# Performance work log

Hardware: AMD Instinct MI355X
Metric: run time of the kernel (lower is better)

Reference implementation:

```python
import jax, jax.numpy as jnp
import numpy as np

B, L = 32, 512
H, W = 352, 1216
MAXLEN = max(H, W)  # max Bresenham path length after clipping to image


def setup_inputs() -> dict:
    key = jax.random.key(0)
    k1, k2 = jax.random.split(key)
    pred = jax.random.normal(k1, (B, 1, H, W), dtype=jnp.float32)
    lines = jax.random.randint(k2, (B, L, 2, 2), 0, 1216, dtype=jnp.int32)
    return {"pred": pred, "lines": lines}


def _bresenham_paths(lines):
    # lines: [B, L, 2, 2] int32, last dim = (x, y), coords already clipped.
    # Closed-form skimage/Bresenham: along the major axis i=0..dmaj,
    # minor_i = min0 + smin * floor((2*dmin*i + dmaj) / (2*dmaj)).
    x0 = lines[..., 0, 0]; y0 = lines[..., 0, 1]
    x1 = lines[..., 1, 0]; y1 = lines[..., 1, 1]
    dx = jnp.abs(x1 - x0); dy = jnp.abs(y1 - y0)
    xmajor = dx > dy  # skimage 'steep' swap: x is major iff |dx| > |dy|
    dmaj = jnp.where(xmajor, dx, dy)
    dmin = jnp.where(xmajor, dy, dx)
    smaj = jnp.where(xmajor, jnp.sign(x1 - x0), jnp.sign(y1 - y0))
    smin = jnp.where(xmajor, jnp.sign(y1 - y0), jnp.sign(x1 - x0))
    maj0 = jnp.where(xmajor, x0, y0)
    min0 = jnp.where(xmajor, y0, x0)
    i = jnp.arange(MAXLEN, dtype=jnp.int32)
    # Clamp step index to dmaj -> padding repeats the endpoint, so diffs there are 0.
    i_eff = jnp.minimum(i[None, None, :], dmaj[..., None])       # [B, L, MAXLEN]
    dmaj_e = dmaj[..., None]
    dmaj_safe = jnp.maximum(dmaj_e, 1)
    maj = maj0[..., None] + smaj[..., None] * i_eff
    minr = min0[..., None] + smin[..., None] * (
        (2 * dmin[..., None] * i_eff + dmaj_e) // (2 * dmaj_safe))
    xs = jnp.where(xmajor[..., None], maj, minr)
    ys = jnp.where(xmajor[..., None], minr, maj)
    return xs, ys


def reference(pred, lines):
    # Clip coords into the image, exactly like the torch module.
    x = jnp.clip(lines[..., 0], 0, W - 1)
    y = jnp.clip(lines[..., 1], 0, H - 1)
    lines_c = jnp.stack([x, y], axis=-1)                          # [B, L, 2, 2]

    xs, ys = _bresenham_paths(lines_c)                            # [B, L, MAXLEN]
    p = pred.reshape(B, H * W)
    idx = (ys * W + xs).reshape(B, -1)
    vals = jnp.take_along_axis(p, idx, axis=1).reshape(B, L, MAXLEN)

    # Sum of |diff| of depth along each line (padding repeats endpoint -> 0 diff).
    diff_sums = jnp.sum(jnp.abs(jnp.diff(vals, axis=-1)), axis=-1)  # [B, L]
    # Skip lines whose endpoint depth gap < 0.5 (data-dependent skip -> mask).
    end_diff = jnp.abs(vals[..., 0] - vals[..., -1])
    diff_sums = jnp.where(end_diff < 0.5, 0.0, diff_sums)

    # Angle-based weights (computed from clipped lines, as in the original).
    lf = lines_c.astype(jnp.float32)
    slopes = jnp.abs((lf[:, :, 1, 1] - lf[:, :, 0, 1]) /
                     (lf[:, :, 1, 0] - lf[:, :, 0, 0] + 1e-6))
    degrees = (jnp.arctan(slopes) * 180.0 / jnp.pi) % 90.0
    mx = jnp.max(degrees, axis=1, keepdims=True)                  # per-sample max
    skew_factor = 1.5
    skewed = degrees ** skew_factor / (mx + 1.0) ** (skew_factor - 1.0)
    sharp = 2.5
    heights = 90.0 - (jnp.abs(skewed - 45.0) ** sharp) ** (1.0 / sharp)
    weights = (heights / 300.0) ** 4

    return jnp.sum(weights * diff_sums)
```

## Files before the change

### kernel.cpp

```cpp
#include <hip/hip_runtime.h>
#include <math.h>

#define BB 32
#define LL 512
#define HH 352
#define WW 1216
#define NLINES (BB * LL)
#define LPW 2
#define NBLK2 (NLINES / (LPW * 4))

typedef float f4 __attribute__((ext_vector_type(4), aligned(4)));

__device__ __forceinline__ float line_degree(int x0, int y0, int x1, int y1) {
    float slope = fabsf(((float)y1 - (float)y0) / ((float)x1 - (float)x0 + 1e-6f));
    float deg = (atanf(slope) * 180.0f) / 3.14159274101257324f;
    return fmodf(deg, 90.0f);
}

__device__ __forceinline__ float walk_line(const float* __restrict__ p, int lane,
        int x0, int y0, int x1, int y1) {
    int dx = abs(x1 - x0), dy = abs(y1 - y0);
    bool xm = dx > dy;
    int dmaj = xm ? dx : dy;
    int dmin = xm ? dy : dx;
    float s = 0.0f;
    if (dy == 0) {
        int base = y0 * WW + min(x0, x1);
        int dxs = dmaj;
        int nch = (dxs + 254) / 255;
        for (int j = 0; j < nch; ++j) {
            int pi0 = j * 255 + (lane << 2);
            int f0 = base + pi0;
            int fc = min(f0, HH * WW - 4);
            f4 v = *(const f4*)(p + fc);
            float nx = __shfl_down(v.x, 1);
            float d0 = fabsf(v.y - v.x);
            float d1 = fabsf(v.z - v.y);
            float d2 = fabsf(v.w - v.z);
            float d3 = fabsf(nx - v.w);
            s += (pi0     < dxs) ? d0 : 0.0f;
            s += (pi0 + 1 < dxs) ? d1 : 0.0f;
            s += (pi0 + 2 < dxs) ? d2 : 0.0f;
            s += (pi0 + 3 < dxs && lane < 63) ? d3 : 0.0f;
        }
    } else {
        int sx = (x1 > x0) - (x1 < x0);
        int sy = (y1 > y0) - (y1 < y0);
        int smaj = xm ? sx : sy;
        int smin = xm ? sy : sx;
        int maj0 = xm ? x0 : y0;
        int min0 = xm ? y0 : x0;
        unsigned den = 2u * (unsigned)dmaj;
        int tdm = 2 * dmin;
        unsigned M = 0xFFFFFFFFu / den + 1u;
        int sA = xm ? 1 : WW;
        int sB = xm ? WW : 1;
        int A = smaj * sA;
        int Bm = smin * sB;
        int off0 = maj0 * sA + min0 * sB;
        int niter = (dmaj + 62) / 63;
        int nbatch = (niter + 7) >> 3;
        int idx = lane;
        for (int t = 0; t < nbatch; ++t, idx += 504) {
            int offs[8];
            #pragma unroll
            for (int k = 0; k < 8; ++k) {
                int idc = min(idx + 63 * k, dmaj);
                unsigned num = (unsigned)(tdm * idc) + (unsigned)dmaj;
                unsigned q = __umulhi(num, M);
                q -= (q * den > num) ? 1u : 0u;
                offs[k] = off0 + idc * A + (int)q * Bm;
            }
            float v[8];
            #pragma unroll
            for (int k = 0; k < 8; ++k) v[k] = p[offs[k]];
            #pragma unroll
            for (int k = 0; k < 8; ++k) {
                float vn = __shfl_down(v[k], 1);
                float d = fabsf(vn - v[k]);
                s += (lane < 63) ? d : 0.0f;
            }
        }
    }
    return s;
}

__global__ void __launch_bounds__(256) line_walk_kernel(
        const float* __restrict__ pred, const int* __restrict__ lines,
        float* __restrict__ partials, unsigned* __restrict__ counter) {
    if (blockIdx.x == 0 && threadIdx.x == 0) *counter = 0;
    int lane = threadIdx.x & 63;
    int w = threadIdx.x >> 6;
    int bid = blockIdx.x;
    int swz = (bid & 7) * (NBLK2 / 8) + (bid >> 3);
    int W = swz * 4 + w;
    int g0 = W * LPW, g1 = g0 + 1;
    int b = g0 >> 9;

    int4 lA = ((const int4*)lines)[g0];
    int4 lB = ((const int4*)lines)[g1];
    int ax0 = min(max(lA.x, 0), WW - 1), ay0 = min(max(lA.y, 0), HH - 1);
    int ax1 = min(max(lA.z, 0), WW - 1), ay1 = min(max(lA.w, 0), HH - 1);
    int bx0 = min(max(lB.x, 0), WW - 1), by0 = min(max(lB.y, 0), HH - 1);
    int bx1 = min(max(lB.z, 0), WW - 1), by1 = min(max(lB.w, 0), HH - 1);

    const float* __restrict__ p = pred + (size_t)b * (HH * WW);

    float vfA = p[ay0 * WW + ax0];
    float vlA = p[ay1 * WW + ax1];
    float vfB = p[by0 * WW + bx0];
    float vlB = p[by1 * WW + bx1];

    int admaj = max(abs(ax1 - ax0), abs(ay1 - ay0));
    int bdmaj = max(abs(bx1 - bx0), abs(by1 - by0));

    bool actA = (fabsf(vfA - vlA) >= 0.5f) && (admaj > 0);
    bool actB = (fabsf(vfB - vlB) >= 0.5f) && (bdmaj > 0);

    float s0 = actA ? walk_line(p, lane, ax0, ay0, ax1, ay1) : 0.0f;
    float s1 = actB ? walk_line(p, lane, bx0, by0, bx1, by1) : 0.0f;

    #pragma unroll
    for (int off = 32; off > 0; off >>= 1) {
        s0 += __shfl_down(s0, off);
        s1 += __shfl_down(s1, off);
    }
    if (lane == 0) {
        partials[g0] = actA ? s0 : 0.0f;
        partials[g1] = actB ? s1 : 0.0f;
    }
}

__global__ void finalize_kernel(const int* __restrict__ lines,
                                const float* __restrict__ partials,
                                float* __restrict__ bsum,
                                unsigned* __restrict__ counter,
                                float* __restrict__ out) {
    __shared__ float wred[8];
    __shared__ float bc;
    int b = blockIdx.x;
    int t = threadIdx.x;
    int lane = t & 63, wv = t >> 6;
    int g = b * LL + t;
    int4 ln = ((const int4*)lines)[g];
    int x0 = min(max(ln.x, 0), WW - 1);
    int y0 = min(max(ln.y, 0), HH - 1);
    int x1 = min(max(ln.z, 0), WW - 1);
    int y1 = min(max(ln.w, 0), HH - 1);
    float deg = line_degree(x0, y0, x1, y1);

    float m = deg;
    #pragma unroll
    for (int off = 32; off > 0; off >>= 1) m = fmaxf(m, __shfl_down(m, off));
    if (lane == 0) wred[wv] = m;
    __syncthreads();
    if (t == 0) {
        float mm = wred[0];
        #pragma unroll
        for (int i = 1; i < 8; ++i) mm = fmaxf(mm, wred[i]);
        bc = mm;
    }
    __syncthreads();
    float mxv = bc;

    float skewed = (deg * sqrtf(deg)) / sqrtf(mxv + 1.0f);
    float tt = fabsf(skewed - 45.0f);
    float h = 90.0f - tt;
    float hw = h * (1.0f / 300.0f);
    float hw2 = hw * hw;
    float wgt = hw2 * hw2;
    float sv = wgt * partials[g];
    #pragma unroll
    for (int off = 32; off > 0; off >>= 1) sv += __shfl_down(sv, off);
    if (lane == 0) wred[wv] = sv;
    __syncthreads();
    if (t == 0) {
        float tot = 0.0f;
        #pragma unroll
        for (int i = 0; i < 8; ++i) tot += wred[i];
        bsum[b] = tot;
        __threadfence();
        if (atomicAdd(counter, 1u) == BB - 1) {
            __threadfence();
            float acc = 0.0f;
            #pragma unroll
            for (int i = 0; i < BB; ++i) acc += bsum[i];
            out[0] = acc;
        }
    }
}

extern "C" void kernel_launch(void* const* d_in, const int* in_sizes, int n_in,
                              void* d_out, int out_size, void* d_ws, size_t ws_size,
                              hipStream_t stream) {
    const float* pred = (const float*)d_in[0];
    const int* lines = (const int*)d_in[1];
    float* out = (float*)d_out;
    float* ws = (float*)d_ws;
    float* partials = ws;
    float* bsum = ws + NLINES;
    unsigned* counter = (unsigned*)(ws + NLINES + BB);

    line_walk_kernel<<<NBLK2, 256, 0, stream>>>(pred, lines, partials, counter);
    finalize_kernel<<<BB, LL, 0, stream>>>(lines, partials, bsum, counter, out);
}
```

Before: 20.75 us.

## Speculatively issue first gather batch before endpoint-skip test to overlap latency

```diff
diff --git a/kernel.cpp b/kernel.cpp
--- a/kernel.cpp
+++ b/kernel.cpp
@@ -8,6 +8,7 @@
 #define NLINES (BB * LL)
 #define LPW 2
 #define NBLK2 (NLINES / (LPW * 4))
+#define MAXOFF (HH * WW - 4)
 
 typedef float f4 __attribute__((ext_vector_type(4), aligned(4)));
 
@@ -17,71 +18,68 @@
     return fmodf(deg, 90.0f);
 }
 
-__device__ __forceinline__ float walk_line(const float* __restrict__ p, int lane,
-        int x0, int y0, int x1, int y1) {
-    int dx = abs(x1 - x0), dy = abs(y1 - y0);
+struct SPar {
+    int off0, A, Bm, tdm, dmaj;
+    unsigned den, M;
+};
+
+__device__ __forceinline__ SPar make_spar(int x0, int y0, int x1, int y1,
+                                          int dx, int dy) {
+    SPar c;
     bool xm = dx > dy;
-    int dmaj = xm ? dx : dy;
+    c.dmaj = xm ? dx : dy;
     int dmin = xm ? dy : dx;
+    int sx = (x1 > x0) - (x1 < x0);
+    int sy = (y1 > y0) - (y1 < y0);
+    int smaj = xm ? sx : sy;
+    int smin = xm ? sy : sx;
+    int maj0 = xm ? x0 : y0;
+    int min0 = xm ? y0 : x0;
+    int sA = xm ? 1 : WW;
+    int sB = xm ? WW : 1;
+    c.A = smaj * sA;
+    c.Bm = smin * sB;
+    c.off0 = maj0 * sA + min0 * sB;
+    c.tdm = 2 * dmin;
+    c.den = 2u * (unsigned)c.dmaj;
+    c.M = 0xFFFFFFFFu / c.den + 1u;
+    return c;
+}
+
+__device__ __forceinline__ void spar_offs(const SPar& c, int idx, int* offs) {
+    #pragma unroll
+    for (int k = 0; k < 8; ++k) {
+        int idc = min(idx + 63 * k, c.dmaj);
+        unsigned num = (unsigned)(c.tdm * idc) + (unsigned)c.dmaj;
+        unsigned q = __umulhi(num, c.M);
+        q -= (q * c.den > num) ? 1u : 0u;
+        offs[k] = c.off0 + idc * c.A + (int)q * c.Bm;
+    }
+}
+
+__device__ __forceinline__ float batch_consume(const float* v, int lane) {
     float s = 0.0f;
-    if (dy == 0) {
-        int base = y0 * WW + min(x0, x1);
-        int dxs = dmaj;
-        int nch = (dxs + 254) / 255;
-        for (int j = 0; j < nch; ++j) {
-            int pi0 = j * 255 + (lane << 2);
-            int f0 = base + pi0;
-            int fc = min(f0, HH * WW - 4);
-            f4 v = *(const f4*)(p + fc);
-            float nx = __shfl_down(v.x, 1);
-            float d0 = fabsf(v.y - v.x);
-            float d1 = fabsf(v.z - v.y);
-            float d2 = fabsf(v.w - v.z);
-            float d3 = fabsf(nx - v.w);
-            s += (pi0     < dxs) ? d0 : 0.0f;
-            s += (pi0 + 1 < dxs) ? d1 : 0.0f;
-            s += (pi0 + 2 < dxs) ? d2 : 0.0f;
-            s += (pi0 + 3 < dxs && lane < 63) ? d3 : 0.0f;
-        }
-    } else {
-        int sx = (x1 > x0) - (x1 < x0);
-        int sy = (y1 > y0) - (y1 < y0);
-        int smaj = xm ? sx : sy;
-        int smin = xm ? sy : sx;
-        int maj0 = xm ? x0 : y0;
-        int min0 = xm ? y0 : x0;
-        unsigned den = 2u * (unsigned)dmaj;
-        int tdm = 2 * dmin;
-        unsigned M = 0xFFFFFFFFu / den + 1u;
-        int sA = xm ? 1 : WW;
-        int sB = xm ? WW : 1;
-        int A = smaj * sA;
-        int Bm = smin * sB;
-        int off0 = maj0 * sA + min0 * sB;
-        int niter = (dmaj + 62) / 63;
-        int nbatch = (niter + 7) >> 3;
-        int idx = lane;
-        for (int t = 0; t < nbatch; ++t, idx += 504) {
-            int offs[8];
-            #pragma unroll
-            for (int k = 0; k < 8; ++k) {
-                int idc = min(idx + 63 * k, dmaj);
-                unsigned num = (unsigned)(tdm * idc) + (unsigned)dmaj;
-                unsigned q = __umulhi(num, M);
-                q -= (q * den > num) ? 1u : 0u;
-                offs[k] = off0 + idc * A + (int)q * Bm;
-            }
-            float v[8];
-            #pragma unroll
-            for (int k = 0; k < 8; ++k) v[k] = p[offs[k]];
-            #pragma unroll
-            for (int k = 0; k < 8; ++k) {
-                float vn = __shfl_down(v[k], 1);
-                float d = fabsf(vn - v[k]);
-                s += (lane < 63) ? d : 0.0f;
-            }
-        }
-    }
+    #pragma unroll
+    for (int k = 0; k < 8; ++k) {
+        float vn = __shfl_down(v[k], 1);
+        float d = fabsf(vn - v[k]);
+        s += (lane < 63) ? d : 0.0f;
+    }
+    return s;
+}
+
+__device__ __forceinline__ float hchunk_consume(f4 v, int lane, int cbase, int dxs) {
+    int pi0 = cbase + (lane << 2);
+    float nx = __shfl_down(v.x, 1);
+    float d0 = fabsf(v.y - v.x);
+    float d1 = fabsf(v.z - v.y);
+    float d2 = fabsf(v.w - v.z);
+    float d3 = fabsf(nx - v.w);
+    float s = 0.0f;
+    s += (pi0     < dxs) ? d0 : 0.0f;
+    s += (pi0 + 1 < dxs) ? d1 : 0.0f;
+    s += (pi0 + 2 < dxs) ? d2 : 0.0f;
+    s += (pi0 + 3 < dxs && lane < 63) ? d3 : 0.0f;
     return s;
 }
 
@@ -106,19 +104,101 @@
 
     const float* __restrict__ p = pred + (size_t)b * (HH * WW);
 
+    int dxA = abs(ax1 - ax0), dyA = abs(ay1 - ay0);
+    int dxB = abs(bx1 - bx0), dyB = abs(by1 - by0);
+    bool hA = (dyA == 0), hB = (dyB == 0);
+
     float vfA = p[ay0 * WW + ax0];
     float vlA = p[ay1 * WW + ax1];
     float vfB = p[by0 * WW + bx0];
     float vlB = p[by1 * WW + bx1];
 
-    int admaj = max(abs(ax1 - ax0), abs(ay1 - ay0));
-    int bdmaj = max(abs(bx1 - bx0), abs(by1 - by0));
-
+    SPar cA, cB;
+    int baseA = 0, dxsA = 0, baseB = 0, dxsB = 0;
+    float vA[8], vB[8];
+    f4 hA0, hA1, hB0, hB1;
+    if (hA) {
+        baseA = ay0 * WW + min(ax0, ax1);
+        dxsA = dxA;
+        hA0 = *(const f4*)(p + min(baseA + (lane << 2), MAXOFF));
+        hA1 = *(const f4*)(p + min(baseA + 255 + (lane << 2), MAXOFF));
+    } else {
+        cA = make_spar(ax0, ay0, ax1, ay1, dxA, dyA);
+        int offs[8];
+        spar_offs(cA, lane, offs);
+        #pragma unroll
+        for (int k = 0; k < 8; ++k) vA[k] = p[offs[k]];
+    }
+    if (hB) {
+        baseB = by0 * WW + min(bx0, bx1);
+        dxsB = dxB;
+        hB0 = *(const f4*)(p + min(baseB + (lane << 2), MAXOFF));
+        hB1 = *(const f4*)(p + min(baseB + 255 + (lane << 2), MAXOFF));
+    } else {
+        cB = make_spar(bx0, by0, bx1, by1, dxB, dyB);
+        int offs[8];
+        spar_offs(cB, lane, offs);
+        #pragma unroll
+        for (int k = 0; k < 8; ++k) vB[k] = p[offs[k]];
+    }
+
+    int admaj = max(dxA, dyA);
+    int bdmaj = max(dxB, dyB);
     bool actA = (fabsf(vfA - vlA) >= 0.5f) && (admaj > 0);
     bool actB = (fabsf(vfB - vlB) >= 0.5f) && (bdmaj > 0);
 
-    float s0 = actA ? walk_line(p, lane, ax0, ay0, ax1, ay1) : 0.0f;
-    float s1 = actB ? walk_line(p, lane, bx0, by0, bx1, by1) : 0.0f;
+    float s0 = 0.0f, s1 = 0.0f;
+    if (hA) {
+        s0 += hchunk_consume(hA0, lane, 0, dxsA);
+        s0 += hchunk_consume(hA1, lane, 255, dxsA);
+    } else {
+        s0 += batch_consume(vA, lane);
+    }
+    if (hB) {
+        s1 += hchunk_consume(hB0, lane, 0, dxsB);
+        s1 += hchunk_consume(hB1, lane, 255, dxsB);
+    } else {
+        s1 += batch_consume(vB, lane);
+    }
+
+    if (actA) {
+        if (hA) {
+            int nch = (dxsA + 254) / 255;
+            for (int j = 2; j < nch; ++j) {
+                f4 v = *(const f4*)(p + min(baseA + j * 255 + (lane << 2), MAXOFF));
+                s0 += hchunk_consume(v, lane, j * 255, dxsA);
+            }
+        } else {
+            int nbatch = (((cA.dmaj + 62) / 63) + 7) >> 3;
+            for (int t = 1; t < nbatch; ++t) {
+                int offs[8];
+                spar_offs(cA, lane + t * 504, offs);
+                float v[8];
+                #pragma unroll
+                for (int k = 0; k < 8; ++k) v[k] = p[offs[k]];
+                s0 += batch_consume(v, lane);
+            }
+        }
+    }
+    if (actB) {
+        if (hB) {
+            int nch = (dxsB + 254) / 255;
+            for (int j = 2; j < nch; ++j) {
+                f4 v = *(const f4*)(p + min(baseB + j * 255 + (lane << 2), MAXOFF));
+                s1 += hchunk_consume(v, lane, j * 255, dxsB);
+            }
+        } else {
+            int nbatch = (((cB.dmaj + 62) / 63) + 7) >> 3;
+            for (int t = 1; t < nbatch; ++t) {
+                int offs[8];
+                spar_offs(cB, lane + t * 504, offs);
+                float v[8];
+                #pragma unroll
+                for (int k = 0; k < 8; ++k) v[k] = p[offs[k]];
+                s1 += batch_consume(v, lane);
+            }
+        }
+    }
 
     #pragma unroll
     for (int off = 32; off > 0; off >>= 1) {
```

After: 22.39 us. 7.9% more time.
